# Kernel tuning notes

Hardware: AMD Instinct MI355X
Metric: run time of the kernel (lower is better)

Reference implementation:

```python
import jax, jax.numpy as jnp
import numpy as np

N_NODES = 100000


def gcn_conv(x, src, dst, w, W, b, n):
    # PyG GCNConv: add self loops (weight 1), symmetric normalization,
    # linear transform, scatter-add aggregation, bias.
    loop = jnp.arange(n, dtype=src.dtype)
    s = jnp.concatenate([src, loop])
    d = jnp.concatenate([dst, loop])
    ew = jnp.concatenate([w, jnp.ones((n,), dtype=w.dtype)])
    deg = jax.ops.segment_sum(ew, d, num_segments=n)          # [N]
    dinv = jnp.where(deg > 0, jax.lax.rsqrt(deg), 0.0).astype(x.dtype)
    norm = dinv[s] * ew * dinv[d]                             # [E+N]
    h = x @ W                                                 # [N, out]
    msg = h[s] * norm[:, None]                                # gather + scale
    out = jax.ops.segment_sum(msg, d, num_segments=n)         # scatter-add
    return out + b


def setup_inputs() -> dict:
    key = jax.random.key(0)
    k1, k2, k3, k4, k5, k6 = jax.random.split(key, 6)
    n, e, c_in, c_hid, c_out = N_NODES, 1200000, 64, 64, 32
    node_matrix = jax.random.normal(k1, (n, c_in), dtype=jnp.float32)
    edge_index = jax.random.randint(k2, (2, e), 0, n, dtype=jnp.int64)
    edge_weights = jax.random.uniform(k3, (e,), dtype=jnp.float32)
    s_in = 1.0 / np.sqrt(c_in)
    s_hid = 1.0 / np.sqrt(c_hid)
    W1 = jax.random.uniform(k4, (c_in, c_hid), jnp.float32, -s_in, s_in)
    b1 = jnp.zeros((c_hid,), jnp.float32)
    W2 = jax.random.uniform(k5, (c_hid, c_out), jnp.float32, -s_hid, s_hid)
    b2 = jnp.zeros((c_out,), jnp.float32)
    return {"node_matrix": node_matrix, "edge_index": edge_index,
            "edge_weights": edge_weights, "W1": W1, "b1": b1, "W2": W2, "b2": b2}


def reference(node_matrix, edge_index, edge_weights, W1, b1, W2, b2):
    n = node_matrix.shape[0]
    src, dst = edge_index[0], edge_index[1]
    x = gcn_conv(node_matrix, src, dst, edge_weights, W1, b1, n)
    x = jax.nn.relu(x)
    x = gcn_conv(x, src, dst, edge_weights, W2, b2, n)
    return x
```

## Files before the change

kernel.cpp:

```cpp
#include <hip/hip_runtime.h>

static inline int ceil_div(long long a, long long b) { return (int)((a + b - 1) / b); }

#define RBITS 8
#define RNODES 256
#define CNT_BLOCKS 96

typedef __attribute__((ext_vector_type(8))) short bf16x8;
typedef __attribute__((ext_vector_type(4))) float f32x4;

__device__ inline unsigned f2bf(float f) {
    unsigned u = __float_as_uint(f);
    return (u + 0x7fffu + ((u >> 16) & 1u)) >> 16;
}
__device__ inline float bf2f(unsigned v) { return __uint_as_float(v << 16); }
__device__ inline float bf_lo(unsigned v) { return __uint_as_float(v << 16); }
__device__ inline float bf_hi(unsigned v) { return __uint_as_float(v & 0xffff0000u); }

__global__ void bin_count(const int* __restrict__ dst, int* __restrict__ hist_g,
                          int NB, int E) {
    __shared__ int hist[512];
    int t = threadIdx.x;
    hist[t] = 0;
    __syncthreads();
    int nvec = E >> 2;
    const int4* d4 = (const int4*)dst;
    for (int v = blockIdx.x * 512 + t; v < nvec; v += CNT_BLOCKS * 512) {
        int4 d = d4[v];
        atomicAdd(&hist[d.x >> RBITS], 1);
        atomicAdd(&hist[d.y >> RBITS], 1);
        atomicAdd(&hist[d.z >> RBITS], 1);
        atomicAdd(&hist[d.w >> RBITS], 1);
    }
    if (blockIdx.x == 0 && t < (E & 3))
        atomicAdd(&hist[dst[(nvec << 2) + t] >> RBITS], 1);
    __syncthreads();
    if (t < NB) hist_g[blockIdx.x * NB + t] = hist[t];
}

__global__ void bin_scan(const int* __restrict__ hist_g, int* __restrict__ bin_start,
                         int* __restrict__ bin_cursor, int NB) {
    __shared__ int s[512];
    int t = threadIdx.x;
    int v = 0;
    if (t < NB) {
        for (int k = 0; k < CNT_BLOCKS; ++k) v += hist_g[k * NB + t];
        bin_cursor[t] = 0;
    }
    s[t] = v;
    __syncthreads();
    for (int d = 1; d < 512; d <<= 1) {
        int a = (t >= d) ? s[t - d] : 0;
        __syncthreads();
        s[t] += a;
        __syncthreads();
    }
    if (t < NB) bin_start[t] = s[t] - v;
    if (t == NB - 1) bin_start[NB] = s[t];
}

#define SC_T 512
#define SC_K 8
#define SC_E (SC_T * SC_K)
__global__ void bin_scatter(const int* __restrict__ src, const int* __restrict__ dst,
                            const float* __restrict__ w, int* __restrict__ bin_cursor,
                            const int* __restrict__ bin_start,
                            int* __restrict__ bp, float* __restrict__ bw,
                            int NB, int E) {
    __shared__ int hist[512];
    __shared__ int offs[512];
    __shared__ int base[512];
    __shared__ int stage_p[SC_E];
    __shared__ float stage_w[SC_E];
    __shared__ unsigned short stage_b[SC_E];
    int t = threadIdx.x;
    hist[t] = 0;
    __syncthreads();
    int e0 = blockIdx.x * SC_E;
    int nE = E - e0; if (nE > SC_E) nE = SC_E;

    int myBin[SC_K], myRank[SC_K], myPack[SC_K];
    float myW[SC_K];
#pragma unroll
    for (int k = 0; k < SC_K; ++k) {
        int idx = t + k * SC_T;
        if (idx < nE) {
            int e = e0 + idx;
            int d = dst[e];
            int b = d >> RBITS;
            myBin[k] = b;
            myPack[k] = (src[e] << RBITS) | (d & (RNODES - 1));
            myW[k] = w[e];
            myRank[k] = atomicAdd(&hist[b], 1);
        }
    }
    __syncthreads();
    offs[t] = hist[t];
    __syncthreads();
    for (int d = 1; d < 512; d <<= 1) {
        int a = (t >= d) ? offs[t - d] : 0;
        __syncthreads();
        offs[t] += a;
        __syncthreads();
    }
    if (t < NB && hist[t]) base[t] = bin_start[t] + atomicAdd(&bin_cursor[t], hist[t]);
#pragma unroll
    for (int k = 0; k < SC_K; ++k) {
        int idx = t + k * SC_T;
        if (idx < nE) {
            int b = myBin[k];
            int pos = (offs[b] - hist[b]) + myRank[k];
            stage_p[pos] = myPack[k];
            stage_w[pos] = myW[k];
            stage_b[pos] = (unsigned short)b;
        }
    }
    __syncthreads();
    for (int p = t; p < nE; p += SC_T) {
        int b = stage_b[p];
        int g = base[b] + (p - (offs[b] - hist[b]));
        bp[g] = stage_p[p];
        bw[g] = stage_w[p];
    }
}

__global__ void csr_build(const int* __restrict__ bp, const float* __restrict__ bw,
                          const int* __restrict__ bin_start,
                          int* __restrict__ row_beg, int* __restrict__ row_cnt,
                          float* __restrict__ dinv,
                          int* __restrict__ fsrc, float* __restrict__ fw,
                          int N, int NB) {
    __shared__ int cnt[RNODES];
    __shared__ float wsum[RNODES];
    __shared__ int starts[RNODES];
    __shared__ int cur[RNODES];
    int b = blockIdx.x;
    int t = threadIdx.x;
    if (t < RNODES) { cnt[t] = 0; wsum[t] = 0.f; }
    __syncthreads();
    int beg = bin_start[b], end = bin_start[b + 1];
    for (int e = beg + t; e < end; e += 512) {
        int off = bp[e] & (RNODES - 1);
        atomicAdd(&cnt[off], 1);
        atomicAdd(&wsum[off], bw[e]);
    }
    __syncthreads();
    if (t < RNODES) starts[t] = cnt[t];
    __syncthreads();
    for (int d = 1; d < RNODES; d <<= 1) {
        int a = 0;
        if (t < RNODES && t >= d) a = starts[t - d];
        __syncthreads();
        if (t < RNODES) starts[t] += a;
        __syncthreads();
    }
    if (t < RNODES) {
        int ex = starts[t] - cnt[t];
        cur[t] = beg + ex;
        int node = (b << RBITS) + t;
        if (node < N) {
            row_beg[node] = beg + ex;
            row_cnt[node] = cnt[t];
            dinv[node] = rsqrtf(wsum[t] + 1.0f);
        }
    }
    __syncthreads();
    for (int e = beg + t; e < end; e += 512) {
        int p = bp[e];
        int slot = atomicAdd(&cur[p & (RNODES - 1)], 1);
        fsrc[slot] = p >> RBITS;
        fw[slot] = bw[e];
    }
}

__global__ __launch_bounds__(256) void gemm1_mfma(const float* __restrict__ X,
                                                  const float* __restrict__ W,
                                                  unsigned short* __restrict__ H, int N) {
    int lane = threadIdx.x & 63;
    int wv = threadIdx.x >> 6;
    int quad = lane >> 4;
    int col = lane & 15;

    bf16x8 Bh[4][2], Bl[4][2];
#pragma unroll
    for (int nt = 0; nt < 4; ++nt)
#pragma unroll
        for (int kh = 0; kh < 2; ++kh)
#pragma unroll
            for (int j = 0; j < 8; ++j) {
                float wval = W[(kh * 32 + quad * 8 + j) * 64 + nt * 16 + col];
                unsigned hb = f2bf(wval);
                Bh[nt][kh][j] = (short)hb;
                Bl[nt][kh][j] = (short)f2bf(wval - bf2f(hb));
            }

#pragma unroll
    for (int rt = 0; rt < 4; ++rt) {
        int rb = blockIdx.x * 256 + wv * 64 + rt * 16;
        if (rb >= N) break;
        int arow = rb + col;
        bf16x8 Ah[2], Al[2];
#pragma unroll
        for (int kh = 0; kh < 2; ++kh) {
            float xv[8];
            if (arow < N) {
                const float4* p = (const float4*)(X + (size_t)arow * 64 + kh * 32 + quad * 8);
                float4 f0 = p[0], f1 = p[1];
                xv[0] = f0.x; xv[1] = f0.y; xv[2] = f0.z; xv[3] = f0.w;
                xv[4] = f1.x; xv[5] = f1.y; xv[6] = f1.z; xv[7] = f1.w;
            } else {
#pragma unroll
                for (int j = 0; j < 8; ++j) xv[j] = 0.f;
            }
#pragma unroll
            for (int j = 0; j < 8; ++j) {
                unsigned hb = f2bf(xv[j]);
                Ah[kh][j] = (short)hb;
                Al[kh][j] = (short)f2bf(xv[j] - bf2f(hb));
            }
        }
        f32x4 acc[4] = {{0,0,0,0},{0,0,0,0},{0,0,0,0},{0,0,0,0}};
#pragma unroll
        for (int nt = 0; nt < 4; ++nt)
#pragma unroll
            for (int kh = 0; kh < 2; ++kh) {
                acc[nt] = __builtin_amdgcn_mfma_f32_16x16x32_bf16(Ah[kh], Bh[nt][kh], acc[nt], 0, 0, 0);
                acc[nt] = __builtin_amdgcn_mfma_f32_16x16x32_bf16(Al[kh], Bh[nt][kh], acc[nt], 0, 0, 0);
                acc[nt] = __builtin_amdgcn_mfma_f32_16x16x32_bf16(Ah[kh], Bl[nt][kh], acc[nt], 0, 0, 0);
            }
#pragma unroll
        for (int nt = 0; nt < 4; ++nt)
#pragma unroll
            for (int r = 0; r < 4; ++r) {
                int row = rb + quad * 4 + r;
                if (row < N)
                    H[(size_t)row * 64 + nt * 16 + col] = (unsigned short)f2bf(acc[nt][r]);
            }
    }
}

__global__ __launch_bounds__(256) void gemm2_mfma(const float* __restrict__ X,
                                                  const float* __restrict__ W,
                                                  unsigned short* __restrict__ H, int N) {
    int lane = threadIdx.x & 63;
    int wv = threadIdx.x >> 6;
    int quad = lane >> 4;
    int col = lane & 15;

    bf16x8 Bh[2][2], Bl[2][2];
#pragma unroll
    for (int nt = 0; nt < 2; ++nt)
#pragma unroll
        for (int kh = 0; kh < 2; ++kh)
#pragma unroll
            for (int j = 0; j < 8; ++j) {
                float wval = W[(kh * 32 + quad * 8 + j) * 32 + nt * 16 + col];
                unsigned hb = f2bf(wval);
                Bh[nt][kh][j] = (short)hb;
                Bl[nt][kh][j] = (short)f2bf(wval - bf2f(hb));
            }

#pragma unroll
    for (int rt = 0; rt < 4; ++rt) {
        int rb = blockIdx.x * 256 + wv * 64 + rt * 16;
        if (rb >= N) break;
        int arow = rb + col;
        bf16x8 Ah[2], Al[2];
#pragma unroll
        for (int kh = 0; kh < 2; ++kh) {
            float xv[8];
            if (arow < N) {
                const float4* p = (const float4*)(X + (size_t)arow * 64 + kh * 32 + quad * 8);
                float4 f0 = p[0], f1 = p[1];
                xv[0] = f0.x; xv[1] = f0.y; xv[2] = f0.z; xv[3] = f0.w;
                xv[4] = f1.x; xv[5] = f1.y; xv[6] = f1.z; xv[7] = f1.w;
            } else {
#pragma unroll
                for (int j = 0; j < 8; ++j) xv[j] = 0.f;
            }
#pragma unroll
            for (int j = 0; j < 8; ++j) {
                float xr = fmaxf(xv[j], 0.f);
                unsigned hb = f2bf(xr);
                Ah[kh][j] = (short)hb;
                Al[kh][j] = (short)f2bf(xr - bf2f(hb));
            }
        }
        f32x4 acc[2] = {{0,0,0,0},{0,0,0,0}};
#pragma unroll
        for (int nt = 0; nt < 2; ++nt)
#pragma unroll
            for (int kh = 0; kh < 2; ++kh) {
                acc[nt] = __builtin_amdgcn_mfma_f32_16x16x32_bf16(Ah[kh], Bh[nt][kh], acc[nt], 0, 0, 0);
                acc[nt] = __builtin_amdgcn_mfma_f32_16x16x32_bf16(Al[kh], Bh[nt][kh], acc[nt], 0, 0, 0);
                acc[nt] = __builtin_amdgcn_mfma_f32_16x16x32_bf16(Ah[kh], Bl[nt][kh], acc[nt], 0, 0, 0);
            }
#pragma unroll
        for (int nt = 0; nt < 2; ++nt)
#pragma unroll
            for (int r = 0; r < 4; ++r) {
                int row = rb + quad * 4 + r;
                if (row < N)
                    H[(size_t)row * 32 + nt * 16 + col] = (unsigned short)f2bf(acc[nt][r]);
            }
    }
}

__global__ void aggregate64(const unsigned* __restrict__ h, const int* __restrict__ row_beg,
                            const int* __restrict__ row_cnt, const int* __restrict__ fsrc,
                            const float* __restrict__ fw, const float* __restrict__ dinv,
                            const float* __restrict__ b, float* __restrict__ out, int N) {
    int t = threadIdx.x;
    int c = t & 7;
    int i = blockIdx.x * 64 + (t >> 3);
    if (i >= N) return;
    int e = row_beg[i];
    int end = e + row_cnt[i];
    const uint4* h4 = (const uint4*)h;
    float acc[8];
#pragma unroll
    for (int j = 0; j < 8; ++j) acc[j] = 0.f;
    for (; e + 3 < end; e += 4) {
        int s0 = fsrc[e], s1 = fsrc[e + 1], s2 = fsrc[e + 2], s3 = fsrc[e + 3];
        float n0 = fw[e] * dinv[s0];
        float n1 = fw[e + 1] * dinv[s1];
        float n2 = fw[e + 2] * dinv[s2];
        float n3 = fw[e + 3] * dinv[s3];
        uint4 v0 = h4[(size_t)s0 * 8 + c];
        uint4 v1 = h4[(size_t)s1 * 8 + c];
        uint4 v2 = h4[(size_t)s2 * 8 + c];
        uint4 v3 = h4[(size_t)s3 * 8 + c];
        acc[0] += n0 * bf_lo(v0.x) + n1 * bf_lo(v1.x) + n2 * bf_lo(v2.x) + n3 * bf_lo(v3.x);
        acc[1] += n0 * bf_hi(v0.x) + n1 * bf_hi(v1.x) + n2 * bf_hi(v2.x) + n3 * bf_hi(v3.x);
        acc[2] += n0 * bf_lo(v0.y) + n1 * bf_lo(v1.y) + n2 * bf_lo(v2.y) + n3 * bf_lo(v3.y);
        acc[3] += n0 * bf_hi(v0.y) + n1 * bf_hi(v1.y) + n2 * bf_hi(v2.y) + n3 * bf_hi(v3.y);
        acc[4] += n0 * bf_lo(v0.z) + n1 * bf_lo(v1.z) + n2 * bf_lo(v2.z) + n3 * bf_lo(v3.z);
        acc[5] += n0 * bf_hi(v0.z) + n1 * bf_hi(v1.z) + n2 * bf_hi(v2.z) + n3 * bf_hi(v3.z);
        acc[6] += n0 * bf_lo(v0.w) + n1 * bf_lo(v1.w) + n2 * bf_lo(v2.w) + n3 * bf_lo(v3.w);
        acc[7] += n0 * bf_hi(v0.w) + n1 * bf_hi(v1.w) + n2 * bf_hi(v2.w) + n3 * bf_hi(v3.w);
    }
    for (; e < end; ++e) {
        int s0 = fsrc[e];
        float n0 = fw[e] * dinv[s0];
        uint4 v0 = h4[(size_t)s0 * 8 + c];
        acc[0] += n0 * bf_lo(v0.x);
        acc[1] += n0 * bf_hi(v0.x);
        acc[2] += n0 * bf_lo(v0.y);
        acc[3] += n0 * bf_hi(v0.y);
        acc[4] += n0 * bf_lo(v0.z);
        acc[5] += n0 * bf_hi(v0.z);
        acc[6] += n0 * bf_lo(v0.w);
        acc[7] += n0 * bf_hi(v0.w);
    }
    float di = dinv[i];
    uint4 hv = h4[(size_t)i * 8 + c];
    float hs[8] = {bf_lo(hv.x), bf_hi(hv.x), bf_lo(hv.y), bf_hi(hv.y),
                   bf_lo(hv.z), bf_hi(hv.z), bf_lo(hv.w), bf_hi(hv.w)};
    float4 b0 = ((const float4*)b)[c * 2];
    float4 b1 = ((const float4*)b)[c * 2 + 1];
    float4 o0, o1;
    o0.x = b0.x + di * (di * hs[0] + acc[0]);
    o0.y = b0.y + di * (di * hs[1] + acc[1]);
    o0.z = b0.z + di * (di * hs[2] + acc[2]);
    o0.w = b0.w + di * (di * hs[3] + acc[3]);
    o1.x = b1.x + di * (di * hs[4] + acc[4]);
    o1.y = b1.y + di * (di * hs[5] + acc[5]);
    o1.z = b1.z + di * (di * hs[6] + acc[6]);
    o1.w = b1.w + di * (di * hs[7] + acc[7]);
    float4* op = (float4*)(out + (size_t)i * 64 + c * 8);
    op[0] = o0;
    op[1] = o1;
}

__global__ void aggregate32(const unsigned* __restrict__ h, const int* __restrict__ row_beg,
                            const int* __restrict__ row_cnt, const int* __restrict__ fsrc,
                            const float* __restrict__ fw, const float* __restrict__ dinv,
                            const float* __restrict__ b, float* __restrict__ out, int N) {
    int t = threadIdx.x;
    int c = t & 3;
    int i = blockIdx.x * 128 + (t >> 2);
    if (i >= N) return;
    int e = row_beg[i];
    int end = e + row_cnt[i];
    const uint4* h4 = (const uint4*)h;
    float acc[8];
#pragma unroll
    for (int j = 0; j < 8; ++j) acc[j] = 0.f;
    for (; e + 3 < end; e += 4) {
        int s0 = fsrc[e], s1 = fsrc[e + 1], s2 = fsrc[e + 2], s3 = fsrc[e + 3];
        float n0 = fw[e] * dinv[s0];
        float n1 = fw[e + 1] * dinv[s1];
        float n2 = fw[e + 2] * dinv[s2];
        float n3 = fw[e + 3] * dinv[s3];
        uint4 v0 = h4[(size_t)s0 * 4 + c];
        uint4 v1 = h4[(size_t)s1 * 4 + c];
        uint4 v2 = h4[(size_t)s2 * 4 + c];
        uint4 v3 = h4[(size_t)s3 * 4 + c];
        acc[0] += n0 * bf_lo(v0.x) + n1 * bf_lo(v1.x) + n2 * bf_lo(v2.x) + n3 * bf_lo(v3.x);
        acc[1] += n0 * bf_hi(v0.x) + n1 * bf_hi(v1.x) + n2 * bf_hi(v2.x) + n3 * bf_hi(v3.x);
        acc[2] += n0 * bf_lo(v0.y) + n1 * bf_lo(v1.y) + n2 * bf_lo(v2.y) + n3 * bf_lo(v3.y);
        acc[3] += n0 * bf_hi(v0.y) + n1 * bf_hi(v1.y) + n2 * bf_hi(v2.y) + n3 * bf_hi(v3.y);
        acc[4] += n0 * bf_lo(v0.z) + n1 * bf_lo(v1.z) + n2 * bf_lo(v2.z) + n3 * bf_lo(v3.z);
        acc[5] += n0 * bf_hi(v0.z) + n1 * bf_hi(v1.z) + n2 * bf_hi(v2.z) + n3 * bf_hi(v3.z);
        acc[6] += n0 * bf_lo(v0.w) + n1 * bf_lo(v1.w) + n2 * bf_lo(v2.w) + n3 * bf_lo(v3.w);
        acc[7] += n0 * bf_hi(v0.w) + n1 * bf_hi(v1.w) + n2 * bf_hi(v2.w) + n3 * bf_hi(v3.w);
    }
    for (; e < end; ++e) {
        int s0 = fsrc[e];
        float n0 = fw[e] * dinv[s0];
        uint4 v0 = h4[(size_t)s0 * 4 + c];
        acc[0] += n0 * bf_lo(v0.x);
        acc[1] += n0 * bf_hi(v0.x);
        acc[2] += n0 * bf_lo(v0.y);
        acc[3] += n0 * bf_hi(v0.y);
        acc[4] += n0 * bf_lo(v0.z);
        acc[5] += n0 * bf_hi(v0.z);
        acc[6] += n0 * bf_lo(v0.w);
        acc[7] += n0 * bf_hi(v0.w);
    }
    float di = dinv[i];
    uint4 hv = h4[(size_t)i * 4 + c];
    float hs[8] = {bf_lo(hv.x), bf_hi(hv.x), bf_lo(hv.y), bf_hi(hv.y),
                   bf_lo(hv.z), bf_hi(hv.z), bf_lo(hv.w), bf_hi(hv.w)};
    float4 b0 = ((const float4*)b)[c * 2];
    float4 b1 = ((const float4*)b)[c * 2 + 1];
    float4 o0, o1;
    o0.x = b0.x + di * (di * hs[0] + acc[0]);
    o0.y = b0.y + di * (di * hs[1] + acc[1]);
    o0.z = b0.z + di * (di * hs[2] + acc[2]);
    o0.w = b0.w + di * (di * hs[3] + acc[3]);
    o1.x = b1.x + di * (di * hs[4] + acc[4]);
    o1.y = b1.y + di * (di * hs[5] + acc[5]);
    o1.z = b1.z + di * (di * hs[6] + acc[6]);
    o1.w = b1.w + di * (di * hs[7] + acc[7]);
    float4* op = (float4*)(out + (size_t)i * 32 + c * 8);
    op[0] = o0;
    op[1] = o1;
}

extern "C" void kernel_launch(void* const* d_in, const int* in_sizes, int n_in,
                              void* d_out, int out_size, void* d_ws, size_t ws_size,
                              hipStream_t stream) {
    const float* x  = (const float*)d_in[0];
    const int* eidx = (const int*)d_in[1];
    const float* w  = (const float*)d_in[2];
    const float* W1 = (const float*)d_in[3];
    const float* b1 = (const float*)d_in[4];
    const float* W2 = (const float*)d_in[5];
    const float* b2 = (const float*)d_in[6];
    float* out = (float*)d_out;

    const int E = in_sizes[2];
    const int N = in_sizes[0] / 64;
    const int* src = eidx;
    const int* dst = eidx + E;
    const int NB = ceil_div(N, RNODES);

    char* ws = (char*)d_ws;
    size_t off = 0;
    auto alloc = [&](size_t bytes) -> void* {
        void* p = ws + off;
        off = (off + bytes + 255) & ~(size_t)255;
        return p;
    };
    int*      hist_g     = (int*)alloc((size_t)CNT_BLOCKS * NB * 4);
    int*      bin_cursor = (int*)alloc((size_t)NB * 4);
    int*      bin_start  = (int*)alloc((size_t)(NB + 1) * 4);
    int*      bp         = (int*)alloc((size_t)E * 4);
    float*    bw         = (float*)alloc((size_t)E * 4);
    int*      fsrc       = (int*)alloc((size_t)E * 4);
    float*    fw         = (float*)alloc((size_t)E * 4);
    int*      row_beg    = (int*)alloc((size_t)N * 4);
    int*      row_cnt    = (int*)alloc((size_t)N * 4);
    float*    dinv       = (float*)alloc((size_t)N * 4);
    unsigned* h1         = (unsigned*)alloc((size_t)N * 32 * 4);
    unsigned* h2         = (unsigned*)alloc((size_t)N * 16 * 4);
    float*    out1       = (float*)alloc((size_t)N * 64 * 4);

    bin_count<<<CNT_BLOCKS, 512, 0, stream>>>(dst, hist_g, NB, E);
    bin_scan<<<1, 512, 0, stream>>>(hist_g, bin_start, bin_cursor, NB);
    bin_scatter<<<ceil_div(E, SC_E), SC_T, 0, stream>>>(src, dst, w, bin_cursor, bin_start,
                                                        bp, bw, NB, E);
    csr_build<<<NB, 512, 0, stream>>>(bp, bw, bin_start, row_beg, row_cnt, dinv, fsrc, fw, N, NB);

    gemm1_mfma<<<ceil_div(N, 256), 256, 0, stream>>>(x, W1, (unsigned short*)h1, N);
    aggregate64<<<ceil_div(N, 64), 512, 0, stream>>>(h1, row_beg, row_cnt, fsrc, fw, dinv, b1, out1, N);

    gemm2_mfma<<<ceil_div(N, 256), 256, 0, stream>>>(out1, W2, (unsigned short*)h2, N);
    aggregate32<<<ceil_div(N, 128), 512, 0, stream>>>(h2, row_beg, row_cnt, fsrc, fw, dinv, b2, out, N);
}
```

Before: 210.4 us.

## Precompute edge norms into packed CSR and store layer-1 output as bf16 with ReLU

Splits CSR construction into a degree pass and a scatter pass so each edge's weight can be pre-multiplied by the source node's dinv and stored with the source index in one uint2. Both aggregation kernels then skip the random dinv gather per edge and read one 8-byte record instead of two arrays. The first aggregation now applies ReLU and writes bf16 instead of fp32, halving that intermediate's traffic, and gemm2 reads bf16 directly and drops the low-part A MFMA. The cost is an extra kernel launch plus a second pass over the binned edges, and lower precision for the layer-1 activations.

```diff
diff --git a/kernel.cpp b/kernel.cpp
--- a/kernel.cpp
+++ b/kernel.cpp
@@ -13,6 +13,7 @@
     unsigned u = __float_as_uint(f);
     return (u + 0x7fffu + ((u >> 16) & 1u)) >> 16;
 }
+__device__ inline unsigned pack2(float a, float b) { return f2bf(a) | (f2bf(b) << 16); }
 __device__ inline float bf2f(unsigned v) { return __uint_as_float(v << 16); }
 __device__ inline float bf_lo(unsigned v) { return __uint_as_float(v << 16); }
 __device__ inline float bf_hi(unsigned v) { return __uint_as_float(v & 0xffff0000u); }
@@ -124,16 +125,13 @@
     }
 }
 
-__global__ void csr_build(const int* __restrict__ bp, const float* __restrict__ bw,
-                          const int* __restrict__ bin_start,
-                          int* __restrict__ row_beg, int* __restrict__ row_cnt,
-                          float* __restrict__ dinv,
-                          int* __restrict__ fsrc, float* __restrict__ fw,
-                          int N, int NB) {
+__global__ void deg_csr(const int* __restrict__ bp, const float* __restrict__ bw,
+                        const int* __restrict__ bin_start,
+                        int* __restrict__ row_beg, int* __restrict__ row_cnt,
+                        float* __restrict__ dinv, int N) {
     __shared__ int cnt[RNODES];
     __shared__ float wsum[RNODES];
     __shared__ int starts[RNODES];
-    __shared__ int cur[RNODES];
     int b = blockIdx.x;
     int t = threadIdx.x;
     if (t < RNODES) { cnt[t] = 0; wsum[t] = 0.f; }
@@ -155,21 +153,35 @@
         __syncthreads();
     }
     if (t < RNODES) {
-        int ex = starts[t] - cnt[t];
-        cur[t] = beg + ex;
         int node = (b << RBITS) + t;
         if (node < N) {
-            row_beg[node] = beg + ex;
+            row_beg[node] = beg + (starts[t] - cnt[t]);
             row_cnt[node] = cnt[t];
             dinv[node] = rsqrtf(wsum[t] + 1.0f);
         }
     }
-    __syncthreads();
+}
+
+__global__ void csr_scatter(const int* __restrict__ bp, const float* __restrict__ bw,
+                            const int* __restrict__ bin_start, const int* __restrict__ row_beg,
+                            const float* __restrict__ dinv, uint2* __restrict__ ew, int N) {
+    __shared__ int cur[RNODES];
+    int b = blockIdx.x;
+    int t = threadIdx.x;
+    if (t < RNODES) {
+        int node = (b << RBITS) + t;
+        cur[t] = (node < N) ? row_beg[node] : 0;
+    }
+    __syncthreads();
+    int beg = bin_start[b], end = bin_start[b + 1];
     for (int e = beg + t; e < end; e += 512) {
         int p = bp[e];
+        int s = p >> RBITS;
         int slot = atomicAdd(&cur[p & (RNODES - 1)], 1);
-        fsrc[slot] = p >> RBITS;
-        fw[slot] = bw[e];
+        uint2 v;
+        v.x = (unsigned)s;
+        v.y = __float_as_uint(bw[e] * dinv[s]);
+        ew[slot] = v;
     }
 }
 
@@ -239,7 +251,7 @@
     }
 }
 
-__global__ __launch_bounds__(256) void gemm2_mfma(const float* __restrict__ X,
+__global__ __launch_bounds__(256) void gemm2_mfma(const unsigned short* __restrict__ Xb,
                                                   const float* __restrict__ W,
                                                   unsigned short* __restrict__ H, int N) {
     int lane = threadIdx.x & 63;
@@ -265,25 +277,14 @@
         int rb = blockIdx.x * 256 + wv * 64 + rt * 16;
         if (rb >= N) break;
         int arow = rb + col;
-        bf16x8 Ah[2], Al[2];
+        bf16x8 A[2];
 #pragma unroll
         for (int kh = 0; kh < 2; ++kh) {
-            float xv[8];
             if (arow < N) {
-                const float4* p = (const float4*)(X + (size_t)arow * 64 + kh * 32 + quad * 8);
-                float4 f0 = p[0], f1 = p[1];
-                xv[0] = f0.x; xv[1] = f0.y; xv[2] = f0.z; xv[3] = f0.w;
-                xv[4] = f1.x; xv[5] = f1.y; xv[6] = f1.z; xv[7] = f1.w;
+                const bf16x8* p = (const bf16x8*)(Xb + (size_t)arow * 64 + kh * 32 + quad * 8);
+                A[kh] = *p;
             } else {
-#pragma unroll
-                for (int j = 0; j < 8; ++j) xv[j] = 0.f;
-            }
-#pragma unroll
-            for (int j = 0; j < 8; ++j) {
-                float xr = fmaxf(xv[j], 0.f);
-                unsigned hb = f2bf(xr);
-                Ah[kh][j] = (short)hb;
-                Al[kh][j] = (short)f2bf(xr - bf2f(hb));
+                A[kh] = bf16x8{0,0,0,0,0,0,0,0};
             }
         }
         f32x4 acc[2] = {{0,0,0,0},{0,0,0,0}};
@@ -291,9 +292,8 @@
         for (int nt = 0; nt < 2; ++nt)
 #pragma unroll
             for (int kh = 0; kh < 2; ++kh) {
-                acc[nt] = __builtin_amdgcn_mfma_f32_16x16x32_bf16(Ah[kh], Bh[nt][kh], acc[nt], 0, 0, 0);
-                acc[nt] = __builtin_amdgcn_mfma_f32_16x16x32_bf16(Al[kh], Bh[nt][kh], acc[nt], 0, 0, 0);
-                acc[nt] = __builtin_amdgcn_mfma_f32_16x16x32_bf16(Ah[kh], Bl[nt][kh], acc[nt], 0, 0, 0);
+                acc[nt] = __builtin_amdgcn_mfma_f32_16x16x32_bf16(A[kh], Bh[nt][kh], acc[nt], 0, 0, 0);
+                acc[nt] = __builtin_amdgcn_mfma_f32_16x16x32_bf16(A[kh], Bl[nt][kh], acc[nt], 0, 0, 0);
             }
 #pragma unroll
         for (int nt = 0; nt < 2; ++nt)
@@ -307,9 +307,9 @@
 }
 
 __global__ void aggregate64(const unsigned* __restrict__ h, const int* __restrict__ row_beg,
-                            const int* __restrict__ row_cnt, const int* __restrict__ fsrc,
-                            const float* __restrict__ fw, const float* __restrict__ dinv,
-                            const float* __restrict__ b, float* __restrict__ out, int N) {
+                            const int* __restrict__ row_cnt, const uint2* __restrict__ ew,
+                            const float* __restrict__ dinv, const float* __restrict__ b,
+                            unsigned* __restrict__ outb, int N) {
     int t = threadIdx.x;
     int c = t & 7;
     int i = blockIdx.x * 64 + (t >> 3);
@@ -321,15 +321,15 @@
 #pragma unroll
     for (int j = 0; j < 8; ++j) acc[j] = 0.f;
     for (; e + 3 < end; e += 4) {
-        int s0 = fsrc[e], s1 = fsrc[e + 1], s2 = fsrc[e + 2], s3 = fsrc[e + 3];
-        float n0 = fw[e] * dinv[s0];
-        float n1 = fw[e + 1] * dinv[s1];
-        float n2 = fw[e + 2] * dinv[s2];
-        float n3 = fw[e + 3] * dinv[s3];
-        uint4 v0 = h4[(size_t)s0 * 8 + c];
-        uint4 v1 = h4[(size_t)s1 * 8 + c];
-        uint4 v2 = h4[(size_t)s2 * 8 + c];
-        uint4 v3 = h4[(size_t)s3 * 8 + c];
+        uint2 e0 = ew[e], e1 = ew[e + 1], e2 = ew[e + 2], e3 = ew[e + 3];
+        float n0 = __uint_as_float(e0.y);
+        float n1 = __uint_as_float(e1.y);
+        float n2 = __uint_as_float(e2.y);
+        float n3 = __uint_as_float(e3.y);
+        uint4 v0 = h4[(size_t)e0.x * 8 + c];
+        uint4 v1 = h4[(size_t)e1.x * 8 + c];
+        uint4 v2 = h4[(size_t)e2.x * 8 + c];
+        uint4 v3 = h4[(size_t)e3.x * 8 + c];
         acc[0] += n0 * bf_lo(v0.x) + n1 * bf_lo(v1.x) + n2 * bf_lo(v2.x) + n3 * bf_lo(v3.x);
         acc[1] += n0 * bf_hi(v0.x) + n1 * bf_hi(v1.x) + n2 * bf_hi(v2.x) + n3 * bf_hi(v3.x);
         acc[2] += n0 * bf_lo(v0.y) + n1 * bf_lo(v1.y) + n2 * bf_lo(v2.y) + n3 * bf_lo(v3.y);
@@ -340,9 +340,9 @@
         acc[7] += n0 * bf_hi(v0.w) + n1 * bf_hi(v1.w) + n2 * bf_hi(v2.w) + n3 * bf_hi(v3.w);
     }
     for (; e < end; ++e) {
-        int s0 = fsrc[e];
-        float n0 = fw[e] * dinv[s0];
-        uint4 v0 = h4[(size_t)s0 * 8 + c];
+        uint2 e0 = ew[e];
+        float n0 = __uint_as_float(e0.y);
+        uint4 v0 = h4[(size_t)e0.x * 8 + c];
         acc[0] += n0 * bf_lo(v0.x);
         acc[1] += n0 * bf_hi(v0.x);
         acc[2] += n0 * bf_lo(v0.y);
@@ -358,24 +358,29 @@
                    bf_lo(hv.z), bf_hi(hv.z), bf_lo(hv.w), bf_hi(hv.w)};
     float4 b0 = ((const float4*)b)[c * 2];
     float4 b1 = ((const float4*)b)[c * 2 + 1];
-    float4 o0, o1;
-    o0.x = b0.x + di * (di * hs[0] + acc[0]);
-    o0.y = b0.y + di * (di * hs[1] + acc[1]);
-    o0.z = b0.z + di * (di * hs[2] + acc[2]);
-    o0.w = b0.w + di * (di * hs[3] + acc[3]);
-    o1.x = b1.x + di * (di * hs[4] + acc[4]);
-    o1.y = b1.y + di * (di * hs[5] + acc[5]);
-    o1.z = b1.z + di * (di * hs[6] + acc[6]);
-    o1.w = b1.w + di * (di * hs[7] + acc[7]);
-    float4* op = (float4*)(out + (size_t)i * 64 + c * 8);
-    op[0] = o0;
-    op[1] = o1;
+    float o[8];
+    o[0] = b0.x + di * (di * hs[0] + acc[0]);
+    o[1] = b0.y + di * (di * hs[1] + acc[1]);
+    o[2] = b0.z + di * (di * hs[2] + acc[2]);
+    o[3] = b0.w + di * (di * hs[3] + acc[3]);
+    o[4] = b1.x + di * (di * hs[4] + acc[4]);
+    o[5] = b1.y + di * (di * hs[5] + acc[5]);
+    o[6] = b1.z + di * (di * hs[6] + acc[6]);
+    o[7] = b1.w + di * (di * hs[7] + acc[7]);
+#pragma unroll
+    for (int j = 0; j < 8; ++j) o[j] = fmaxf(o[j], 0.f);
+    uint4 ov;
+    ov.x = pack2(o[0], o[1]);
+    ov.y = pack2(o[2], o[3]);
+    ov.z = pack2(o[4], o[5]);
+    ov.w = pack2(o[6], o[7]);
+    ((uint4*)outb)[(size_t)i * 8 + c] = ov;
 }
 
 __global__ void aggregate32(const unsigned* __restrict__ h, const int* __restrict__ row_beg,
-                            const int* __restrict__ row_cnt, const int* __restrict__ fsrc,
-                            const float* __restrict__ fw, const float* __restrict__ dinv,
-                            const float* __restrict__ b, float* __restrict__ out, int N) {
+                            const int* __restrict__ row_cnt, const uint2* __restrict__ ew,
+                            const float* __restrict__ dinv, const float* __restrict__ b,
+                            float* __restrict__ out, int N) {
     int t = threadIdx.x;
     int c = t & 3;
     int i = blockIdx.x * 128 + (t >> 2);
@@ -387,15 +392,15 @@
 #pragma unroll
     for (int j = 0; j < 8; ++j) acc[j] = 0.f;
     for (; e + 3 < end; e += 4) {
-        int s0 = fsrc[e], s1 = fsrc[e + 1], s2 = fsrc[e + 2], s3 = fsrc[e + 3];
-        float n0 = fw[e] * dinv[s0];
-        float n1 = fw[e + 1] * dinv[s1];
-        float n2 = fw[e + 2] * dinv[s2];
-        float n3 = fw[e + 3] * dinv[s3];
-        uint4 v0 = h4[(size_t)s0 * 4 + c];
-        uint4 v1 = h4[(size_t)s1 * 4 + c];
-        uint4 v2 = h4[(size_t)s2 * 4 + c];
-        uint4 v3 = h4[(size_t)s3 * 4 + c];
+        uint2 e0 = ew[e], e1 = ew[e + 1], e2 = ew[e + 2], e3 = ew[e + 3];
+        float n0 = __uint_as_float(e0.y);
+        float n1 = __uint_as_float(e1.y);
+        float n2 = __uint_as_float(e2.y);
+        float n3 = __uint_as_float(e3.y);
+        uint4 v0 = h4[(size_t)e0.x * 4 + c];
+        uint4 v1 = h4[(size_t)e1.x * 4 + c];
+        uint4 v2 = h4[(size_t)e2.x * 4 + c];
+        uint4 v3 = h4[(size_t)e3.x * 4 + c];
         acc[0] += n0 * bf_lo(v0.x) + n1 * bf_lo(v1.x) + n2 * bf_lo(v2.x) + n3 * bf_lo(v3.x);
         acc[1] += n0 * bf_hi(v0.x) + n1 * bf_hi(v1.x) + n2 * bf_hi(v2.x) + n3 * bf_hi(v3.x);
         acc[2] += n0 * bf_lo(v0.y) + n1 * bf_lo(v1.y) + n2 * bf_lo(v2.y) + n3 * bf_lo(v3.y);
@@ -406,9 +411,9 @@
         acc[7] += n0 * bf_hi(v0.w) + n1 * bf_hi(v1.w) + n2 * bf_hi(v2.w) + n3 * bf_hi(v3.w);
     }
     for (; e < end; ++e) {
-        int s0 = fsrc[e];
-        float n0 = fw[e] * dinv[s0];
-        uint4 v0 = h4[(size_t)s0 * 4 + c];
+        uint2 e0 = ew[e];
+        float n0 = __uint_as_float(e0.y);
+        uint4 v0 = h4[(size_t)e0.x * 4 + c];
         acc[0] += n0 * bf_lo(v0.x);
         acc[1] += n0 * bf_hi(v0.x);
         acc[2] += n0 * bf_lo(v0.y);
@@ -468,24 +473,25 @@
     int*      bin_start  = (int*)alloc((size_t)(NB + 1) * 4);
     int*      bp         = (int*)alloc((size_t)E * 4);
     float*    bw         = (float*)alloc((size_t)E * 4);
-    int*      fsrc       = (int*)alloc((size_t)E * 4);
-    float*    fw         = (float*)alloc((size_t)E * 4);
+    uint2*    ew         = (uint2*)alloc((size_t)E * 8);
     int*      row_beg    = (int*)alloc((size_t)N * 4);
     int*      row_cnt    = (int*)alloc((size_t)N * 4);
     float*    dinv       = (float*)alloc((size_t)N * 4);
     unsigned* h1         = (unsigned*)alloc((size_t)N * 32 * 4);
+    unsigned* out1b      = (unsigned*)alloc((size_t)N * 32 * 4);
     unsigned* h2         = (unsigned*)alloc((size_t)N * 16 * 4);
-    float*    out1       = (float*)alloc((size_t)N * 64 * 4);
 
     bin_count<<<CNT_BLOCKS, 512, 0, stream>>>(dst, hist_g, NB, E);
     bin_scan<<<1, 512, 0, stream>>>(hist_g, bin_start, bin_cursor, NB);
     bin_scatter<<<ceil_div(E, SC_E), SC_T, 0, stream>>>(src, dst, w, bin_cursor, bin_start,
                                                         bp, bw, NB, E);
-    csr_build<<<NB, 512, 0, stream>>>(bp, bw, bin_start, row_beg, row_cnt, dinv, fsrc, fw, N, NB);
+    deg_csr<<<NB, 512, 0, stream>>>(bp, bw, bin_start, row_beg, row_cnt, dinv, N);
+    csr_scatter<<<NB, 512, 0, stream>>>(bp, bw, bin_start, row_beg, dinv, ew, N);
 
     gemm1_mfma<<<ceil_div(N, 256), 256, 0, stream>>>(x, W1, (unsigned short*)h1, N);
-    aggregate64<<<ceil_div(N, 64), 512, 0, stream>>>(h1, row_beg, row_cnt, fsrc, fw, dinv, b1, out1, N);
-
-    gemm2_mfma<<<ceil_div(N, 256), 256, 0, stream>>>(out1, W2, (unsigned short*)h2, N);
-    aggregate32<<<ceil_div(N, 128), 512, 0, stream>>>(h2, row_beg, row_cnt, fsrc, fw, dinv, b2, out, N);
-}
+    aggregate64<<<ceil_div(N, 64), 512, 0, stream>>>(h1, row_beg, row_cnt, ew, dinv, b1, out1b, N);
+
+    gemm2_mfma<<<ceil_div(N, 256), 256, 0, stream>>>((const unsigned short*)out1b, W2,
+                                                     (unsigned short*)h2, N);
+    aggregate32<<<ceil_div(N, 128), 512, 0, stream>>>(h2, row_beg, row_cnt, ew, dinv, b2, out, N);
+}
```

Result: faster. 201.9 us (median of 2 runs) (-4.1%).
